# Performance work log

Measured on AMD Instinct MI355X. Metric: run time of the kernel, lower is better.

The kernel has to match this reference:

```python
import jax, jax.numpy as jnp
import numpy as np


def setup_inputs() -> dict:
    key = jax.random.key(0)
    ks = jax.random.split(key, 5)
    B, S, H, I = 8, 2048, 1024, 4096
    # int8 quantized activation / weights / int8 bias, held as int32 for portability
    hidden_states = jax.random.randint(ks[0], (B, S, H), -128, 128, dtype=jnp.int32)
    w_fc = jax.random.randint(ks[1], (H, I), -128, 128, dtype=jnp.int32)   # Conv1D weight [in, out]
    b_fc = jax.random.randint(ks[2], (I,), -128, 128, dtype=jnp.int32)     # int8 bias (B8)
    w_proj = jax.random.randint(ks[3], (I, H), -128, 128, dtype=jnp.int32)
    b_proj = jax.random.normal(ks[4], (H,), dtype=jnp.float32)             # fp32 bias (BFP32)
    alpha_fc = jnp.float32(0.004)   # (x_scale * w_scale / out_scale) of c_fc
    beta_fc = jnp.float32(0.02)     # bias_scale / out_scale of c_fc
    alpha_proj = jnp.float32(0.003) # x_scale * w_scale of c_proj (dequant to fp32)
    return {
        "hidden_states": hidden_states,
        "w_fc": w_fc, "b_fc": b_fc, "alpha_fc": alpha_fc, "beta_fc": beta_fc,
        "w_proj": w_proj, "b_proj": b_proj, "alpha_proj": alpha_proj,
    }


def reference(hidden_states, w_fc, b_fc, alpha_fc, beta_fc, w_proj, b_proj, alpha_proj):
    # ---- c_fc: W8A8B8O8 Conv1D + fused ReLU + requantization to int8 ----
    acc1 = jnp.matmul(hidden_states, w_fc)                       # [B,S,I] int32
    h = acc1.astype(jnp.float32) * alpha_fc + b_fc.astype(jnp.float32) * beta_fc
    h = jax.nn.relu(h)
    # requantize to int8 (round + saturate)
    h_q = jnp.clip(jnp.round(h), -128.0, 127.0).astype(jnp.int32)  # [B,S,I]
    # ---- c_proj: W8A8BFP32OFP32 Conv1D (dequant to fp32) ----
    acc2 = jnp.matmul(h_q, w_proj)                               # [B,S,H] int32
    out = acc2.astype(jnp.float32) * alpha_proj + b_proj
    # dropout is identity in eval mode
    return out
```

## Files before the change

### kernel.cpp

```cpp
#include <hip/hip_runtime.h>
#include <cstdint>
#include <cstddef>

typedef int int4v __attribute__((ext_vector_type(4)));
typedef signed char schar;

#define DEVI __device__ __forceinline__

DEVI void load_lds16(const void* g, void* l) {
  __builtin_amdgcn_global_load_lds(
      (const __attribute__((address_space(1))) void*)g,
      (__attribute__((address_space(3))) void*)l, 16, 0, 0);
}

#define SB0() __builtin_amdgcn_sched_barrier(0)
#define BAR() __builtin_amdgcn_s_barrier()
#define LGKM(n)                                                   \
  do {                                                            \
    asm volatile("s_waitcnt lgkmcnt(" #n ")" ::: "memory");       \
    SB0();                                                        \
  } while (0)
#define VMW(n)                                                    \
  do {                                                            \
    asm volatile("s_waitcnt vmcnt(" #n ")" ::: "memory");         \
    SB0();                                                        \
  } while (0)

__global__ __launch_bounds__(256) void pack_i8(const int* __restrict__ src,
                                               signed char* __restrict__ dst,
                                               int n4) {
  int i = blockIdx.x * 256 + threadIdx.x;
  if (i >= n4) return;
  int4v v = ((const int4v*)src)[i];
  int p = (v.x & 255) | ((v.y & 255) << 8) | ((v.z & 255) << 16) | (v.w << 24);
  ((int*)dst)[i] = p;
}

__global__ __launch_bounds__(256) void pack_wT(const int* __restrict__ w,
                                               signed char* __restrict__ wT,
                                               int K, int N) {
  __shared__ signed char t[64][68];
  int n0 = blockIdx.x * 64, k0 = blockIdx.y * 64;
  int tr = threadIdx.x >> 6, tc = threadIdx.x & 63;
#pragma unroll
  for (int i = 0; i < 16; ++i) {
    int r = i * 4 + tr;
    t[r][tc] = (signed char)w[(size_t)(k0 + r) * N + n0 + tc];
  }
  __syncthreads();
#pragma unroll
  for (int i = 0; i < 16; ++i) {
    int r = i * 4 + tr;
    wT[(size_t)(n0 + r) * K + k0 + tc] = t[tc][r];
  }
}

template <int EPI>
__global__ __launch_bounds__(512, 2) void gemmR(
    const schar* __restrict__ A, const schar* __restrict__ BT,
    int M, int N, int K, const int* __restrict__ bias_i,
    const float* __restrict__ alphaP, const float* __restrict__ betaP,
    const float* __restrict__ bias_f, schar* __restrict__ outQ,
    float* __restrict__ outF) {
  extern __shared__ schar lds[];

  const int tid = threadIdx.x;
  const int wid = tid >> 6, lane = tid & 63;
  const int wr = wid >> 2, wc = wid & 3;
  const int l16 = lane & 15, l4 = lane >> 4;

  const int gx = gridDim.x;
  const int nwg = gx * gridDim.y;
  const int bid = blockIdx.y * gx + blockIdx.x;
  const int swz = (bid & 7) * (nwg >> 3) + (bid >> 3);
  const int rowBase = (swz / gx) * 256;
  const int colBase = (swz % gx) * 256;
  const int NT = K >> 7;

  const float alpha = alphaP[0];
  const float beta = (EPI == 0) ? betaP[0] : 0.f;
  asm volatile("" ::"s"(alpha), "s"(beta));
  LGKM(0);

  const schar* gA[4];
  const schar* gB[4];
#pragma unroll
  for (int c = 0; c < 4; ++c) {
    int off = c * 8192 + tid * 16;
    int r = off >> 7;
    int gs = ((off >> 4) & 7) ^ (r & 7);
    gA[c] = A + (size_t)(rowBase + r) * K + gs * 16;
    gB[c] = BT + (size_t)(colBase + r) * K + gs * 16;
  }

  auto stage = [&](int buf, int t) {
#pragma unroll
    for (int c = 0; c < 4; ++c)
      load_lds16(gA[c] + (size_t)t * 128,
                 lds + buf * 32768 + c * 8192 + wid * 1024);
#pragma unroll
    for (int c = 0; c < 4; ++c)
      load_lds16(gB[c] + (size_t)t * 128,
                 lds + 65536 + buf * 32768 + c * 8192 + wid * 1024);
  };

  const int so0 = ((0 + l4) ^ (l16 & 7)) * 16 + l16 * 128;
  const int so1 = ((4 + l4) ^ (l16 & 7)) * 16 + l16 * 128;

  int4v acc[8][4] = {};
  int4v aF[8], bF[4];

#define RDA(SO, Ab)                                                  \
  _Pragma("unroll") for (int mi = 0; mi < 8; ++mi) aF[mi] =          \
      *(const int4v*)((Ab) + wr * 16384 + mi * 2048 + (SO))
#define RDB(SO, Bb)                                                  \
  _Pragma("unroll") for (int ni = 0; ni < 4; ++ni) bF[ni] =          \
      *(const int4v*)((Bb) + wc * 8192 + ni * 2048 + (SO))
#define MMALL()                                                      \
  do {                                                               \
    __builtin_amdgcn_s_setprio(1);                                   \
    _Pragma("unroll") for (int mi = 0; mi < 8; ++mi)                 \
        _Pragma("unroll") for (int ni = 0; ni < 4; ++ni) acc[mi][ni] = \
        __builtin_amdgcn_mfma_i32_16x16x64_i8(aF[mi], bF[ni],        \
                                              acc[mi][ni], 0, 0, 0); \
    __builtin_amdgcn_s_setprio(0);                                   \
  } while (0)

  stage(0, 0);
  VMW(0);
  BAR();

  for (int T = 0; T < NT; ++T) {
    const int cb = T & 1, ob = cb ^ 1;
    const schar* Ab = lds + cb * 32768;
    const schar* Bb = lds + 65536 + cb * 32768;

    RDA(so0, Ab);
    RDB(so0, Bb);
    if (T + 1 < NT) stage(ob, T + 1);
    LGKM(0);
    MMALL();
    RDA(so1, Ab);
    RDB(so1, Bb);
    LGKM(0);
    MMALL();

    VMW(0);
    BAR();
  }

  if (EPI == 0) {
#pragma unroll
    for (int MI = 0; MI < 8; ++MI) {
      int row = rowBase + wr * 128 + MI * 16 + l4 * 4;
#pragma unroll
      for (int NI = 0; NI < 4; ++NI) {
        int col = colBase + wc * 64 + NI * 16 + l16;
        float bt = (float)bias_i[col] * beta;
#pragma unroll
        for (int j = 0; j < 4; ++j) {
          float h = (float)acc[MI][NI][j] * alpha + bt;
          h = fmaxf(h, 0.f);
          h = rintf(h);
          h = fminf(h, 127.f);
          outQ[(size_t)(row + j) * N + col] = (schar)h;
        }
      }
    }
  } else {
#pragma unroll
    for (int MI = 0; MI < 8; ++MI) {
      int row = rowBase + wr * 128 + MI * 16 + l4 * 4;
#pragma unroll
      for (int NI = 0; NI < 4; ++NI) {
        int col = colBase + wc * 64 + NI * 16 + l16;
        float bv = bias_f[col];
#pragma unroll
        for (int j = 0; j < 4; ++j)
          outF[(size_t)(row + j) * N + col] =
              (float)acc[MI][NI][j] * alpha + bv;
      }
    }
  }
#undef RDA
#undef RDB
#undef MMALL
}

extern "C" void kernel_launch(void* const* d_in, const int* in_sizes, int n_in,
                              void* d_out, int out_size, void* d_ws,
                              size_t ws_size, hipStream_t stream) {
  const int M = 16384, H = 1024, I = 4096;
  const int* hidden = (const int*)d_in[0];
  const int* w_fc = (const int*)d_in[1];
  const int* b_fc = (const int*)d_in[2];
  const float* alpha_fc = (const float*)d_in[3];
  const float* beta_fc = (const float*)d_in[4];
  const int* w_proj = (const int*)d_in[5];
  const float* b_proj = (const float*)d_in[6];
  const float* alpha_proj = (const float*)d_in[7];
  float* out = (float*)d_out;

  signed char* hq = (signed char*)d_ws;
  signed char* aP = hq + (size_t)M * I;
  signed char* wfcT = aP + (size_t)M * H;
  signed char* wpT = wfcT + (size_t)I * H;

  hipFuncSetAttribute((const void*)gemmR<0>,
                      hipFuncAttributeMaxDynamicSharedMemorySize, 131072);
  hipFuncSetAttribute((const void*)gemmR<1>,
                      hipFuncAttributeMaxDynamicSharedMemorySize, 131072);

  pack_i8<<<(M * H / 4 + 255) / 256, 256, 0, stream>>>(hidden, aP, M * H / 4);
  pack_wT<<<dim3(I / 64, H / 64), 256, 0, stream>>>(w_fc, wfcT, H, I);
  pack_wT<<<dim3(H / 64, I / 64), 256, 0, stream>>>(w_proj, wpT, I, H);

  gemmR<0><<<dim3(I / 256, M / 256), 512, 131072, stream>>>(
      aP, wfcT, M, I, H, b_fc, alpha_fc, beta_fc, nullptr, hq, nullptr);
  gemmR<1><<<dim3(H / 256, M / 256), 512, 131072, stream>>>(
      hq, wpT, M, H, I, nullptr, alpha_proj, nullptr, b_proj, nullptr, out);
}
```

Before: 174.6 us.

## Switch GEMM to 4-stage LDS ring with K-tile 64 and two-ahead prefetch

Cuts the K tile from 128 to 64 bytes and reorganizes the 128KB of LDS into a four-slot ring buffer, so global-to-LDS loads are issued two iterations ahead. The wait only drains down to the newest stage. The LDS swizzle changes to match the 64-byte rows. The aim is to hide global load latency behind MFMA work instead of fully draining vmcnt every iteration. In exchange there are twice as many loop iterations and barriers, and less MFMA work per barrier.

```diff
diff --git a/kernel.cpp b/kernel.cpp
--- a/kernel.cpp
+++ b/kernel.cpp
@@ -56,7 +56,7 @@
 }
 
 template <int EPI>
-__global__ __launch_bounds__(512, 2) void gemmR(
+__global__ __launch_bounds__(512, 2) void gemmP(
     const schar* __restrict__ A, const schar* __restrict__ BT,
     int M, int N, int K, const int* __restrict__ bias_i,
     const float* __restrict__ alphaP, const float* __restrict__ betaP,
@@ -75,77 +75,74 @@
   const int swz = (bid & 7) * (nwg >> 3) + (bid >> 3);
   const int rowBase = (swz / gx) * 256;
   const int colBase = (swz % gx) * 256;
-  const int NT = K >> 7;
+  const int NT = K >> 6;
 
   const float alpha = alphaP[0];
   const float beta = (EPI == 0) ? betaP[0] : 0.f;
   asm volatile("" ::"s"(alpha), "s"(beta));
   LGKM(0);
 
-  const schar* gA[4];
-  const schar* gB[4];
-#pragma unroll
-  for (int c = 0; c < 4; ++c) {
-    int off = c * 8192 + tid * 16;
-    int r = off >> 7;
-    int gs = ((off >> 4) & 7) ^ (r & 7);
-    gA[c] = A + (size_t)(rowBase + r) * K + gs * 16;
-    gB[c] = BT + (size_t)(colBase + r) * K + gs * 16;
+  const schar* gA[2];
+  const schar* gB[2];
+#pragma unroll
+  for (int c = 0; c < 2; ++c) {
+    int o = c * 8192 + tid * 16;
+    int r = o >> 6;
+    int g = ((o >> 4) & 3) ^ ((r >> 1) & 3);
+    gA[c] = A + (size_t)(rowBase + r) * K + g * 16;
+    gB[c] = BT + (size_t)(colBase + r) * K + g * 16;
   }
 
   auto stage = [&](int buf, int t) {
-#pragma unroll
-    for (int c = 0; c < 4; ++c)
-      load_lds16(gA[c] + (size_t)t * 128,
-                 lds + buf * 32768 + c * 8192 + wid * 1024);
-#pragma unroll
-    for (int c = 0; c < 4; ++c)
-      load_lds16(gB[c] + (size_t)t * 128,
-                 lds + 65536 + buf * 32768 + c * 8192 + wid * 1024);
+    schar* d = lds + buf * 32768 + wid * 1024;
+    load_lds16(gA[0] + (size_t)t * 64, d);
+    load_lds16(gA[1] + (size_t)t * 64, d + 8192);
+    load_lds16(gB[0] + (size_t)t * 64, d + 16384);
+    load_lds16(gB[1] + (size_t)t * 64, d + 24576);
   };
 
-  const int so0 = ((0 + l4) ^ (l16 & 7)) * 16 + l16 * 128;
-  const int so1 = ((4 + l4) ^ (l16 & 7)) * 16 + l16 * 128;
+  const int slotc = (l4 ^ ((l16 >> 1) & 3)) * 16 + l16 * 64;
 
   int4v acc[8][4] = {};
   int4v aF[8], bF[4];
 
-#define RDA(SO, Ab)                                                  \
-  _Pragma("unroll") for (int mi = 0; mi < 8; ++mi) aF[mi] =          \
-      *(const int4v*)((Ab) + wr * 16384 + mi * 2048 + (SO))
-#define RDB(SO, Bb)                                                  \
-  _Pragma("unroll") for (int ni = 0; ni < 4; ++ni) bF[ni] =          \
-      *(const int4v*)((Bb) + wc * 8192 + ni * 2048 + (SO))
-#define MMALL()                                                      \
-  do {                                                               \
-    __builtin_amdgcn_s_setprio(1);                                   \
-    _Pragma("unroll") for (int mi = 0; mi < 8; ++mi)                 \
+#define RDA(Ab)                                                   \
+  _Pragma("unroll") for (int mi = 0; mi < 8; ++mi) aF[mi] =       \
+      *(const int4v*)((Ab) + wr * 8192 + mi * 1024 + slotc)
+#define RDB(Bb)                                                   \
+  _Pragma("unroll") for (int ni = 0; ni < 4; ++ni) bF[ni] =       \
+      *(const int4v*)((Bb) + wc * 4096 + ni * 1024 + slotc)
+#define MMALL()                                                        \
+  do {                                                                 \
+    __builtin_amdgcn_s_setprio(1);                                     \
+    _Pragma("unroll") for (int mi = 0; mi < 8; ++mi)                   \
         _Pragma("unroll") for (int ni = 0; ni < 4; ++ni) acc[mi][ni] = \
-        __builtin_amdgcn_mfma_i32_16x16x64_i8(aF[mi], bF[ni],        \
-                                              acc[mi][ni], 0, 0, 0); \
-    __builtin_amdgcn_s_setprio(0);                                   \
+        __builtin_amdgcn_mfma_i32_16x16x64_i8(aF[mi], bF[ni],          \
+                                              acc[mi][ni], 0, 0, 0);   \
+    __builtin_amdgcn_s_setprio(0);                                     \
   } while (0)
 
   stage(0, 0);
-  VMW(0);
+  stage(1, 1);
+  VMW(4);
   BAR();
 
   for (int T = 0; T < NT; ++T) {
-    const int cb = T & 1, ob = cb ^ 1;
+    const int cb = T & 3;
     const schar* Ab = lds + cb * 32768;
-    const schar* Bb = lds + 65536 + cb * 32768;
-
-    RDA(so0, Ab);
-    RDB(so0, Bb);
-    if (T + 1 < NT) stage(ob, T + 1);
+    const schar* Bb = Ab + 16384;
+
+    if (T + 2 < NT) stage((T + 2) & 3, T + 2);
+    RDA(Ab);
+    RDB(Bb);
+    MMALL();
+
     LGKM(0);
-    MMALL();
-    RDA(so1, Ab);
-    RDB(so1, Bb);
-    LGKM(0);
-    MMALL();
-
-    VMW(0);
+    if (T + 2 < NT) {
+      VMW(4);
+    } else {
+      VMW(0);
+    }
     BAR();
   }
 
@@ -206,17 +203,17 @@
   signed char* wfcT = aP + (size_t)M * H;
   signed char* wpT = wfcT + (size_t)I * H;
 
-  hipFuncSetAttribute((const void*)gemmR<0>,
+  hipFuncSetAttribute((const void*)gemmP<0>,
                       hipFuncAttributeMaxDynamicSharedMemorySize, 131072);
-  hipFuncSetAttribute((const void*)gemmR<1>,
+  hipFuncSetAttribute((const void*)gemmP<1>,
                       hipFuncAttributeMaxDynamicSharedMemorySize, 131072);
 
   pack_i8<<<(M * H / 4 + 255) / 256, 256, 0, stream>>>(hidden, aP, M * H / 4);
   pack_wT<<<dim3(I / 64, H / 64), 256, 0, stream>>>(w_fc, wfcT, H, I);
   pack_wT<<<dim3(H / 64, I / 64), 256, 0, stream>>>(w_proj, wpT, I, H);
 
-  gemmR<0><<<dim3(I / 256, M / 256), 512, 131072, stream>>>(
+  gemmP<0><<<dim3(I / 256, M / 256), 512, 131072, stream>>>(
       aP, wfcT, M, I, H, b_fc, alpha_fc, beta_fc, nullptr, hq, nullptr);
-  gemmR<1><<<dim3(H / 256, M / 256), 512, 131072, stream>>>(
+  gemmP<1><<<dim3(H / 256, M / 256), 512, 131072, stream>>>(
       hq, wpT, M, H, I, nullptr, alpha_proj, nullptr, b_proj, nullptr, out);
 }
```

New measurement: 187.1 us. 7.2% more time.

## Drop manual sched barriers and let compiler interleave LDS reads with MFMAs

Applied to the files above, without the earlier changes.

Removes the sched_barrier and memory clobbers from the waitcnt macros and drops the s_setprio bracketing around the MFMA block. Global-to-LDS staging now issues first, both halves of B fragments are loaded into separate registers, and A reads for the second half no longer wait behind an explicit lgkmcnt. The aim is to let the compiler schedule LDS reads alongside MFMAs rather than serialising them. The risk is that, without clobbers, the inline waitcnts no longer order memory operations, so correctness relies on the compiler inserting its own waits, and register pressure rises.

```diff
diff --git a/kernel.cpp b/kernel.cpp
--- a/kernel.cpp
+++ b/kernel.cpp
@@ -13,18 +13,9 @@
       (__attribute__((address_space(3))) void*)l, 16, 0, 0);
 }
 
-#define SB0() __builtin_amdgcn_sched_barrier(0)
 #define BAR() __builtin_amdgcn_s_barrier()
-#define LGKM(n)                                                   \
-  do {                                                            \
-    asm volatile("s_waitcnt lgkmcnt(" #n ")" ::: "memory");       \
-    SB0();                                                        \
-  } while (0)
-#define VMW(n)                                                    \
-  do {                                                            \
-    asm volatile("s_waitcnt vmcnt(" #n ")" ::: "memory");         \
-    SB0();                                                        \
-  } while (0)
+#define LGKM(n) asm volatile("s_waitcnt lgkmcnt(" #n ")")
+#define VMW(n) asm volatile("s_waitcnt vmcnt(" #n ")")
 
 __global__ __launch_bounds__(256) void pack_i8(const int* __restrict__ src,
                                                signed char* __restrict__ dst,
@@ -56,7 +47,7 @@
 }
 
 template <int EPI>
-__global__ __launch_bounds__(512, 2) void gemmR(
+__global__ __launch_bounds__(512, 2) void gemmZ(
     const schar* __restrict__ A, const schar* __restrict__ BT,
     int M, int N, int K, const int* __restrict__ bias_i,
     const float* __restrict__ alphaP, const float* __restrict__ betaP,
@@ -108,23 +99,19 @@
   const int so1 = ((4 + l4) ^ (l16 & 7)) * 16 + l16 * 128;
 
   int4v acc[8][4] = {};
-  int4v aF[8], bF[4];
+  int4v aF[8], bF0[4], bF1[4];
 
 #define RDA(SO, Ab)                                                  \
   _Pragma("unroll") for (int mi = 0; mi < 8; ++mi) aF[mi] =          \
       *(const int4v*)((Ab) + wr * 16384 + mi * 2048 + (SO))
-#define RDB(SO, Bb)                                                  \
-  _Pragma("unroll") for (int ni = 0; ni < 4; ++ni) bF[ni] =          \
+#define RDB(DST, SO, Bb)                                             \
+  _Pragma("unroll") for (int ni = 0; ni < 4; ++ni) (DST)[ni] =       \
       *(const int4v*)((Bb) + wc * 8192 + ni * 2048 + (SO))
-#define MMALL()                                                      \
-  do {                                                               \
-    __builtin_amdgcn_s_setprio(1);                                   \
-    _Pragma("unroll") for (int mi = 0; mi < 8; ++mi)                 \
-        _Pragma("unroll") for (int ni = 0; ni < 4; ++ni) acc[mi][ni] = \
-        __builtin_amdgcn_mfma_i32_16x16x64_i8(aF[mi], bF[ni],        \
-                                              acc[mi][ni], 0, 0, 0); \
-    __builtin_amdgcn_s_setprio(0);                                   \
-  } while (0)
+#define MMALL(BF)                                                      \
+  _Pragma("unroll") for (int mi = 0; mi < 8; ++mi)                     \
+      _Pragma("unroll") for (int ni = 0; ni < 4; ++ni) acc[mi][ni] =   \
+      __builtin_amdgcn_mfma_i32_16x16x64_i8(aF[mi], (BF)[ni],          \
+                                            acc[mi][ni], 0, 0, 0)
 
   stage(0, 0);
   VMW(0);
@@ -135,16 +122,16 @@
     const schar* Ab = lds + cb * 32768;
     const schar* Bb = lds + 65536 + cb * 32768;
 
+    if (T + 1 < NT) stage(ob, T + 1);
+
+    RDB(bF0, so0, Bb);
+    RDB(bF1, so1, Bb);
     RDA(so0, Ab);
-    RDB(so0, Bb);
-    if (T + 1 < NT) stage(ob, T + 1);
+    MMALL(bF0);
+    RDA(so1, Ab);
+    MMALL(bF1);
+
     LGKM(0);
-    MMALL();
-    RDA(so1, Ab);
-    RDB(so1, Bb);
-    LGKM(0);
-    MMALL();
-
     VMW(0);
     BAR();
   }
@@ -206,17 +193,17 @@
   signed char* wfcT = aP + (size_t)M * H;
   signed char* wpT = wfcT + (size_t)I * H;
 
-  hipFuncSetAttribute((const void*)gemmR<0>,
+  hipFuncSetAttribute((const void*)gemmZ<0>,
                       hipFuncAttributeMaxDynamicSharedMemorySize, 131072);
-  hipFuncSetAttribute((const void*)gemmR<1>,
+  hipFuncSetAttribute((const void*)gemmZ<1>,
                       hipFuncAttributeMaxDynamicSharedMemorySize, 131072);
 
   pack_i8<<<(M * H / 4 + 255) / 256, 256, 0, stream>>>(hidden, aP, M * H / 4);
   pack_wT<<<dim3(I / 64, H / 64), 256, 0, stream>>>(w_fc, wfcT, H, I);
   pack_wT<<<dim3(H / 64, I / 64), 256, 0, stream>>>(w_proj, wpT, I, H);
 
-  gemmR<0><<<dim3(I / 256, M / 256), 512, 131072, stream>>>(
+  gemmZ<0><<<dim3(I / 256, M / 256), 512, 131072, stream>>>(
       aP, wfcT, M, I, H, b_fc, alpha_fc, beta_fc, nullptr, hq, nullptr);
-  gemmR<1><<<dim3(H / 256, M / 256), 512, 131072, stream>>>(
+  gemmZ<1><<<dim3(H / 256, M / 256), 512, 131072, stream>>>(
       hq, wpT, M, H, I, nullptr, alpha_proj, nullptr, b_proj, nullptr, out);
 }
```

Measured after the change: 175.9 us. About the same (+0.8%).
